# Optimization experiments

Measured on AMD Instinct MI355X. Metric: run time of the kernel, lower is better.

Reference implementation:

```python
import jax, jax.numpy as jnp
import numpy as np

DIM = 512
HEADS = 8


def setup_inputs() -> dict:
    key = jax.random.key(0)
    k1, k2, k3 = jax.random.split(key, 3)
    x = jax.random.normal(k1, (4, DIM, 64, 64), dtype=jnp.float32)
    # kaiming_normal fan_out, linear: std = 1/sqrt(fan_out)
    w_qkv = jax.random.normal(k2, (3 * DIM, DIM), dtype=jnp.float32) / np.sqrt(3 * DIM)
    b_qkv = jnp.zeros((3 * DIM,), dtype=jnp.float32)
    w_proj = jax.random.normal(k3, (DIM, DIM), dtype=jnp.float32) / np.sqrt(DIM)
    b_proj = jnp.zeros((DIM,), dtype=jnp.float32)
    return {"x": x, "w_qkv": w_qkv, "b_qkv": b_qkv, "w_proj": w_proj, "b_proj": b_proj}


def reference(x, w_qkv, b_qkv, w_proj, b_proj):
    B, C, H, W = x.shape
    N = H * W
    hd = C // HEADS
    scale = hd ** -0.5
    x_flat = x.reshape(B, C, N).transpose(0, 2, 1)          # [B, N, C]
    qkv = x_flat @ w_qkv.T + b_qkv                           # [B, N, 3C]
    q, k, v = jnp.split(qkv, 3, axis=-1)
    q = q.reshape(B, N, HEADS, hd).transpose(0, 2, 1, 3)     # [B, h, N, d]
    k = k.reshape(B, N, HEADS, hd).transpose(0, 2, 1, 3)
    v = v.reshape(B, N, HEADS, hd).transpose(0, 2, 1, 3)
    attn = jnp.einsum('bhnd,bhmd->bhnm', q, k) * scale       # [B, h, N, N]
    attn = jnp.clip(attn, -10.0, 10.0)
    attn = jax.nn.softmax(attn, axis=-1)
    out = jnp.einsum('bhnm,bhmd->bhnd', attn, v)             # [B, h, N, d]
    out = out.transpose(0, 2, 1, 3).reshape(B, N, C)         # [B, N, C]
    out = out @ w_proj.T + b_proj
    out = out.transpose(0, 2, 1).reshape(B, C, H, W)
    return x + out
```

## Files before the change

### kernel.cpp

```cpp
#include <hip/hip_runtime.h>

typedef float f32x4 __attribute__((ext_vector_type(4)));
typedef __bf16 bf16x8 __attribute__((ext_vector_type(8)));
typedef unsigned short u16;
typedef unsigned int u32;
typedef u16 u16x4 __attribute__((ext_vector_type(4)));
typedef u16 u16x8 __attribute__((ext_vector_type(8)));

#define DEV static __device__ __forceinline__

constexpr int B = 4, C = 512, NH = 8, HD = 64, NN = 4096, C3 = 1536;
constexpr float K_PRESCALE = 0.125f * 1.4426950408889634f;
constexpr float CLIP2 = 10.0f * 1.4426950408889634f;

DEV u16 f2bf(float f) { union { __bf16 b; u16 s; } u; u.b = (__bf16)f; return u.s; }

__global__ __launch_bounds__(256) void k_transpose(const float* __restrict__ x,
                                                   u16* __restrict__ Xt) {
  __shared__ float tile[64][65];
  const int n0 = blockIdx.x * 64, c0 = blockIdx.y * 64, b = blockIdx.z;
  const int t = threadIdx.x;
  const int cl = t >> 4, n4 = (t & 15) * 4;
#pragma unroll
  for (int rep = 0; rep < 4; ++rep) {
    const int c = rep * 16 + cl;
    const f32x4 v = *(const f32x4*)(x + ((size_t)(b * C + c0 + c)) * NN + n0 + n4);
#pragma unroll
    for (int j = 0; j < 4; ++j) tile[c][n4 + j] = v[j];
  }
  __syncthreads();
#pragma unroll
  for (int rep = 0; rep < 16; ++rep) {
    const int n = rep * 4 + (t >> 6);
    const int c = t & 63;
    Xt[((size_t)(b * NN + n0 + n)) * C + c0 + c] = f2bf(tile[c][n]);
  }
}

__global__ __launch_bounds__(256) void k_cvtw(const float* __restrict__ wq,
                                              const float* __restrict__ wp,
                                              u16* __restrict__ Wq, u16* __restrict__ Wp) {
  const int idx = blockIdx.x * 256 + threadIdx.x;
  const int NQ = C3 * C / 4;
  const float* src;
  u16* dst;
  int i4;
  if (idx < NQ) { src = wq; dst = Wq; i4 = idx; }
  else          { src = wp; dst = Wp; i4 = idx - NQ; }
  const f32x4 v = *(const f32x4*)(src + (size_t)i4 * 4);
  u16x4 o;
#pragma unroll
  for (int j = 0; j < 4; ++j) o[j] = f2bf(v[j]);
  *(u16x4*)(dst + (size_t)i4 * 4) = o;
}

__global__ __launch_bounds__(256) void k_qkv(const u16* __restrict__ Xt,
                                             const u16* __restrict__ W,
                                             const float* __restrict__ bias,
                                             u16* __restrict__ Q, u16* __restrict__ Kq,
                                             u16* __restrict__ Vt) {
  __shared__ u16 smem[16384];
  u16* Alds = smem;
  u16* Blds = smem + 8192;
  const int nt = blockIdx.x, mt = blockIdx.y, b = blockIdx.z;
  const int t = threadIdx.x, w = t >> 6, l = t & 63;
  const int l15 = l & 15, l4 = l >> 4;
  const int wr = w >> 1, wc = w & 1;
  f32x4 acc[4][4] = {};
  const u16* Abase = Xt + (size_t)(b * NN + nt * 128) * C;
  const u16* Bbase = W + (size_t)(mt * 128) * C;

  for (int kt = 0; kt < C / 64; ++kt) {
    __syncthreads();
#pragma unroll
    for (int i = 0; i < 4; ++i) {
      const int cch = t + 256 * i;
      const int r = cch >> 3, kb = (cch & 7) * 16;
      const int sw = kb ^ ((r & 7) << 4);
      *(f32x4*)((char*)Alds + r * 128 + sw) =
          *(const f32x4*)((const char*)(Abase + (size_t)r * C + kt * 64) + kb);
      *(f32x4*)((char*)Blds + r * 128 + sw) =
          *(const f32x4*)((const char*)(Bbase + (size_t)r * C + kt * 64) + kb);
    }
    __syncthreads();
#pragma unroll
    for (int ks = 0; ks < 2; ++ks) {
      bf16x8 af[4], bfr[4];
#pragma unroll
      for (int ri = 0; ri < 4; ++ri) {
        const int row = wr * 64 + ri * 16 + l15;
        af[ri] = *(const bf16x8*)((const char*)Alds + row * 128 +
                                  ((ks * 64 + l4 * 16) ^ ((row & 7) << 4)));
      }
#pragma unroll
      for (int cj = 0; cj < 4; ++cj) {
        const int row = wc * 64 + cj * 16 + l15;
        bfr[cj] = *(const bf16x8*)((const char*)Blds + row * 128 +
                                   ((ks * 64 + l4 * 16) ^ ((row & 7) << 4)));
      }
#pragma unroll
      for (int ri = 0; ri < 4; ++ri)
#pragma unroll
        for (int cj = 0; cj < 4; ++cj)
          acc[ri][cj] = __builtin_amdgcn_mfma_f32_16x16x32_bf16(af[ri], bfr[cj], acc[ri][cj], 0, 0, 0);
    }
  }

  __syncthreads();
  const int sec = mt >> 2;
  const int mtl = mt & 3;
  if (sec < 2) {
#pragma unroll
    for (int ri = 0; ri < 4; ++ri)
#pragma unroll
      for (int cj = 0; cj < 4; ++cj) {
        const int m_l = wc * 64 + cj * 16 + l15;
        const float bv = bias[mt * 128 + m_l];
        const float sc = (sec == 1) ? K_PRESCALE : 1.0f;
#pragma unroll
        for (int r = 0; r < 4; ++r) {
          const int n_l = wr * 64 + ri * 16 + l4 * 4 + r;
          *(u16*)((char*)smem + n_l * 256 + ((m_l * 2) ^ ((n_l & 7) << 4))) =
              f2bf((acc[ri][cj][r] + bv) * sc);
        }
      }
    __syncthreads();
    u16* dst = (sec == 0) ? Q : Kq;
#pragma unroll
    for (int rep = 0; rep < 8; ++rep) {
      const int idx = rep * 256 + t;
      const int n_l = idx >> 4, ch = idx & 15;
      const u16x8 v = *(const u16x8*)((char*)smem + n_l * 256 + ((ch * 16) ^ ((n_l & 7) << 4)));
      const int hh = mtl * 2 + (ch >> 3), dd = (ch & 7) * 8;
      *(u16x8*)(dst + ((size_t)(b * NH + hh) * NN + nt * 128 + n_l) * HD + dd) = v;
    }
  } else {
#pragma unroll
    for (int ri = 0; ri < 4; ++ri)
#pragma unroll
      for (int cj = 0; cj < 4; ++cj) {
        const int m_l = wc * 64 + cj * 16 + l15;
        const float bv = bias[mt * 128 + m_l];
        const int nb = wr * 64 + ri * 16 + l4 * 4;
        u16x4 pv;
#pragma unroll
        for (int r = 0; r < 4; ++r) pv[r] = f2bf(acc[ri][cj][r] + bv);
        *(u16x4*)((char*)smem + m_l * 256 + ((nb * 2) ^ ((m_l & 7) << 4))) = pv;
      }
    __syncthreads();
#pragma unroll
    for (int rep = 0; rep < 8; ++rep) {
      const int idx = rep * 256 + t;
      const int m_l = idx >> 4, ch = idx & 15;
      const u16x8 v = *(const u16x8*)((char*)smem + m_l * 256 + ((ch * 16) ^ ((m_l & 7) << 4)));
      const int hh = mtl * 2 + (m_l >> 6), dd = m_l & 63;
      *(u16x8*)(Vt + ((size_t)(b * NH + hh) * HD + dd) * NN + nt * 128 + ch * 8) = v;
    }
  }
}

__global__ __launch_bounds__(256) void k_attn(const u16* __restrict__ Q,
                                              const u16* __restrict__ K,
                                              const u16* __restrict__ Vt,
                                              u16* __restrict__ AO) {
  __shared__ u16 Klds[4096];
  __shared__ u16 Vlds[4096];
  __shared__ u16 Plds[4096];
  const int qt = blockIdx.x, h = blockIdx.y, b = blockIdx.z;
  const int bh = b * NH + h;
  const int t = threadIdx.x, w = t >> 6, l = t & 63;
  const int l15 = l & 15, l4 = l >> 4;
  const int q0 = qt * 64;

  const u16* qb = Q + ((size_t)bh * NN + q0 + w * 16 + l15) * HD + l4 * 8;
  bf16x8 qf[2];
  qf[0] = *(const bf16x8*)(qb);
  qf[1] = *(const bf16x8*)(qb + 32);

  f32x4 o[4] = {};
  float rs[4] = {};

  const int sr = t >> 3, scb = (t & 7) * 16;
  const int ssw = scb ^ ((sr & 7) << 4);
  char* kwp = (char*)Klds + sr * 128 + ssw;
  char* vwp = (char*)Vlds + sr * 128 + ssw;
  const char* kg = (const char*)(K + (size_t)bh * NN * HD) + sr * 128 + scb;
  const char* vg = (const char*)(Vt + (size_t)bh * HD * NN) + (size_t)sr * 8192 + scb;

  const int sw7 = (l15 & 7) << 4;

  for (int kv = 0; kv < NN / 64; ++kv) {
    __syncthreads();
    *(f32x4*)kwp          = *(const f32x4*)kg;
    *(f32x4*)(kwp + 4096) = *(const f32x4*)(kg + 4096);
    *(f32x4*)vwp          = *(const f32x4*)vg;
    *(f32x4*)(vwp + 4096) = *(const f32x4*)(vg + (size_t)32 * 8192);
    __syncthreads();

    f32x4 s[4] = {};
#pragma unroll
    for (int ks = 0; ks < 2; ++ks) {
#pragma unroll
      for (int cj = 0; cj < 4; ++cj) {
        const bf16x8 kf = *(const bf16x8*)((const char*)Klds + (cj * 16 + l15) * 128 +
                                           ((ks * 64 + l4 * 16) ^ sw7));
        s[cj] = __builtin_amdgcn_mfma_f32_16x16x32_bf16(qf[ks], kf, s[cj], 0, 0, 0);
      }
    }
#pragma unroll
    for (int cj = 0; cj < 4; ++cj) {
      const int colb = (cj * 16 + l15) * 2;
#pragma unroll
      for (int r = 0; r < 4; ++r) {
        const float p = exp2f(fminf(fmaxf(s[cj][r], -CLIP2), CLIP2));
        rs[r] += p;
        const int row = w * 16 + l4 * 4 + r;
        *(u16*)((char*)Plds + row * 128 + (colb ^ ((row & 7) << 4))) = f2bf(p);
      }
    }
    __syncthreads();

#pragma unroll
    for (int ks = 0; ks < 2; ++ks) {
      const int prow = w * 16 + l15;
      const bf16x8 pa = *(const bf16x8*)((const char*)Plds + prow * 128 +
                                         ((ks * 64 + l4 * 16) ^ sw7));
#pragma unroll
      for (int cj = 0; cj < 4; ++cj) {
        const bf16x8 vf = *(const bf16x8*)((const char*)Vlds + (cj * 16 + l15) * 128 +
                                           ((ks * 64 + l4 * 16) ^ sw7));
        o[cj] = __builtin_amdgcn_mfma_f32_16x16x32_bf16(pa, vf, o[cj], 0, 0, 0);
      }
    }
    kg += 8192;
    vg += 128;
  }

#pragma unroll
  for (int r = 0; r < 4; ++r) {
    float v = rs[r];
    v += __shfl_xor(v, 1);
    v += __shfl_xor(v, 2);
    v += __shfl_xor(v, 4);
    v += __shfl_xor(v, 8);
    rs[r] = v;
  }
#pragma unroll
  for (int cj = 0; cj < 4; ++cj)
#pragma unroll
    for (int r = 0; r < 4; ++r) {
      const int n = q0 + w * 16 + l4 * 4 + r;
      const int c = h * 64 + cj * 16 + l15;
      AO[((size_t)(b * NN + n)) * C + c] = f2bf(o[cj][r] / rs[r]);
    }
}

__global__ __launch_bounds__(256) void k_proj(const u16* __restrict__ AO,
                                              const u16* __restrict__ Wp,
                                              const float* __restrict__ bias,
                                              const float* __restrict__ x,
                                              float* __restrict__ out) {
  __shared__ u16 smem[16384];
  u16* Alds = smem;
  u16* Blds = smem + 8192;
  const int nt = blockIdx.x, ct = blockIdx.y, b = blockIdx.z;
  const int t = threadIdx.x, w = t >> 6, l = t & 63;
  const int l15 = l & 15, l4 = l >> 4;
  const int wr = w >> 1, wc = w & 1;
  f32x4 acc[4][4] = {};
  const u16* Abase = AO + (size_t)(b * NN + nt * 128) * C;
  const u16* Bbase = Wp + (size_t)(ct * 128) * C;

  for (int kt = 0; kt < C / 64; ++kt) {
    __syncthreads();
#pragma unroll
    for (int i = 0; i < 4; ++i) {
      const int cch = t + 256 * i;
      const int r = cch >> 3, kb = (cch & 7) * 16;
      const int sw = kb ^ ((r & 7) << 4);
      *(f32x4*)((char*)Alds + r * 128 + sw) =
          *(const f32x4*)((const char*)(Abase + (size_t)r * C + kt * 64) + kb);
      *(f32x4*)((char*)Blds + r * 128 + sw) =
          *(const f32x4*)((const char*)(Bbase + (size_t)r * C + kt * 64) + kb);
    }
    __syncthreads();
#pragma unroll
    for (int ks = 0; ks < 2; ++ks) {
      bf16x8 af[4], bfr[4];
#pragma unroll
      for (int ri = 0; ri < 4; ++ri) {
        const int row = wr * 64 + ri * 16 + l15;
        af[ri] = *(const bf16x8*)((const char*)Alds + row * 128 +
                                  ((ks * 64 + l4 * 16) ^ ((row & 7) << 4)));
      }
#pragma unroll
      for (int cj = 0; cj < 4; ++cj) {
        const int row = wc * 64 + cj * 16 + l15;
        bfr[cj] = *(const bf16x8*)((const char*)Blds + row * 128 +
                                   ((ks * 64 + l4 * 16) ^ ((row & 7) << 4)));
      }
#pragma unroll
      for (int ri = 0; ri < 4; ++ri)
#pragma unroll
        for (int cj = 0; cj < 4; ++cj)
          acc[ri][cj] = __builtin_amdgcn_mfma_f32_16x16x32_bf16(af[ri], bfr[cj], acc[ri][cj], 0, 0, 0);
    }
  }

  float* fs = (float*)smem;
  __syncthreads();
#pragma unroll
  for (int p = 0; p < 2; ++p) {
    if (p) __syncthreads();
    if (wc == p) {
#pragma unroll
      for (int ri = 0; ri < 4; ++ri)
#pragma unroll
        for (int cj = 0; cj < 4; ++cj) {
          const int co = cj * 16 + l15;
          const float bv = bias[ct * 128 + p * 64 + co];
          const int nb = wr * 64 + ri * 16 + l4 * 4;
          f32x4 vv;
#pragma unroll
          for (int r = 0; r < 4; ++r) vv[r] = acc[ri][cj][r] + bv;
          *(f32x4*)((char*)fs + co * 512 + ((nb * 4) ^ ((co & 7) << 4))) = vv;
        }
    }
    __syncthreads();
#pragma unroll
    for (int rep = 0; rep < 8; ++rep) {
      const int idx = rep * 256 + t;
      const int co = idx >> 5, ch = idx & 31;
      f32x4 vv = *(const f32x4*)((char*)fs + co * 512 + ((ch * 16) ^ ((co & 7) << 4)));
      const size_t base = ((size_t)(b * C + ct * 128 + p * 64 + co)) * NN + nt * 128 + ch * 4;
      const f32x4 xr = *(const f32x4*)(x + base);
#pragma unroll
      for (int r = 0; r < 4; ++r) vv[r] += xr[r];
      *(f32x4*)(out + base) = vv;
    }
  }
}

extern "C" void kernel_launch(void* const* d_in, const int* in_sizes, int n_in,
                              void* d_out, int out_size, void* d_ws, size_t ws_size,
                              hipStream_t stream) {
  const float* x      = (const float*)d_in[0];
  const float* w_qkv  = (const float*)d_in[1];
  const float* b_qkv  = (const float*)d_in[2];
  const float* w_proj = (const float*)d_in[3];
  const float* b_proj = (const float*)d_in[4];
  float* out = (float*)d_out;
  char* ws = (char*)d_ws;

  const size_t SZ_XT = (size_t)B * NN * C * 2;
  const size_t SZ_WQ = (size_t)C3 * C * 2;
  const size_t SZ_WP = (size_t)C * C * 2;
  const size_t SZ_QK = (size_t)B * NH * NN * HD * 2;

  u16* Xt = (u16*)(ws);
  u16* Wq = (u16*)(ws + SZ_XT);
  u16* Wp = (u16*)(ws + SZ_XT + SZ_WQ);
  u16* Qb = (u16*)(ws + SZ_XT + SZ_WQ + SZ_WP);
  u16* Kb = (u16*)(ws + SZ_XT + SZ_WQ + SZ_WP + SZ_QK);
  u16* Vt = (u16*)(ws + SZ_XT + SZ_WQ + SZ_WP + 2 * SZ_QK);
  u16* AO = Xt;

  k_transpose<<<dim3(NN / 64, C / 64, B), 256, 0, stream>>>(x, Xt);
  k_cvtw<<<dim3((C3 * C + C * C) / 4 / 256), 256, 0, stream>>>(w_qkv, w_proj, Wq, Wp);
  k_qkv<<<dim3(NN / 128, C3 / 128, B), 256, 0, stream>>>(Xt, Wq, b_qkv, Qb, Kb, Vt);
  k_attn<<<dim3(NN / 64, NH, B), 256, 0, stream>>>(Qb, Kb, Vt, AO);
  k_proj<<<dim3(NN / 128, C / 128, B), 256, 0, stream>>>(AO, Wp, b_proj, x, out);
}
```

Before: 433.8 us.

## Prefetch next KV tile into registers and compute row sums via MFMA

```diff
diff --git a/kernel.cpp b/kernel.cpp
--- a/kernel.cpp
+++ b/kernel.cpp
@@ -14,6 +14,18 @@
 constexpr float CLIP2 = 10.0f * 1.4426950408889634f;
 
 DEV u16 f2bf(float f) { union { __bf16 b; u16 s; } u; u.b = (__bf16)f; return u.s; }
+
+#if __has_builtin(__builtin_amdgcn_exp2f)
+DEV float fast_exp2(float x) { return __builtin_amdgcn_exp2f(x); }
+#else
+DEV float fast_exp2(float x) { return __expf(x * 0.6931471805599453f); }
+#endif
+
+#if __has_builtin(__builtin_amdgcn_fmed3f)
+DEV float clamp2(float x) { return __builtin_amdgcn_fmed3f(x, -CLIP2, CLIP2); }
+#else
+DEV float clamp2(float x) { return fminf(fmaxf(x, -CLIP2), CLIP2); }
+#endif
 
 __global__ __launch_bounds__(256) void k_transpose(const float* __restrict__ x,
                                                    u16* __restrict__ Xt) {
@@ -177,8 +189,14 @@
   qf[0] = *(const bf16x8*)(qb);
   qf[1] = *(const bf16x8*)(qb + 32);
 
+  union { u16 s; __bf16 b; } ob;
+  ob.s = 0x3F80;
+  bf16x8 ones;
+#pragma unroll
+  for (int j = 0; j < 8; ++j) ones[j] = ob.b;
+
   f32x4 o[4] = {};
-  float rs[4] = {};
+  f32x4 rsa = {};
 
   const int sr = t >> 3, scb = (t & 7) * 16;
   const int ssw = scb ^ ((sr & 7) << 4);
@@ -189,13 +207,26 @@
 
   const int sw7 = (l15 & 7) << 4;
 
-  for (int kv = 0; kv < NN / 64; ++kv) {
-    __syncthreads();
-    *(f32x4*)kwp          = *(const f32x4*)kg;
-    *(f32x4*)(kwp + 4096) = *(const f32x4*)(kg + 4096);
-    *(f32x4*)vwp          = *(const f32x4*)vg;
-    *(f32x4*)(vwp + 4096) = *(const f32x4*)(vg + (size_t)32 * 8192);
-    __syncthreads();
+  f32x4 kr0 = *(const f32x4*)kg;
+  f32x4 kr1 = *(const f32x4*)(kg + 4096);
+  f32x4 vr0 = *(const f32x4*)vg;
+  f32x4 vr1 = *(const f32x4*)(vg + (size_t)32 * 8192);
+  *(f32x4*)kwp = kr0;
+  *(f32x4*)(kwp + 4096) = kr1;
+  *(f32x4*)vwp = vr0;
+  *(f32x4*)(vwp + 4096) = vr1;
+  __syncthreads();
+
+  constexpr int NT = NN / 64;
+  for (int kv = 0; kv < NT; ++kv) {
+    if (kv + 1 < NT) {
+      kg += 8192;
+      vg += 128;
+      kr0 = *(const f32x4*)kg;
+      kr1 = *(const f32x4*)(kg + 4096);
+      vr0 = *(const f32x4*)vg;
+      vr1 = *(const f32x4*)(vg + (size_t)32 * 8192);
+    }
 
     f32x4 s[4] = {};
 #pragma unroll
@@ -212,8 +243,7 @@
       const int colb = (cj * 16 + l15) * 2;
 #pragma unroll
       for (int r = 0; r < 4; ++r) {
-        const float p = exp2f(fminf(fmaxf(s[cj][r], -CLIP2), CLIP2));
-        rs[r] += p;
+        const float p = fast_exp2(clamp2(s[cj][r]));
         const int row = w * 16 + l4 * 4 + r;
         *(u16*)((char*)Plds + row * 128 + (colb ^ ((row & 7) << 4))) = f2bf(p);
       }
@@ -231,27 +261,29 @@
                                            ((ks * 64 + l4 * 16) ^ sw7));
         o[cj] = __builtin_amdgcn_mfma_f32_16x16x32_bf16(pa, vf, o[cj], 0, 0, 0);
       }
-    }
-    kg += 8192;
-    vg += 128;
-  }
-
-#pragma unroll
-  for (int r = 0; r < 4; ++r) {
-    float v = rs[r];
-    v += __shfl_xor(v, 1);
-    v += __shfl_xor(v, 2);
-    v += __shfl_xor(v, 4);
-    v += __shfl_xor(v, 8);
-    rs[r] = v;
-  }
+      rsa = __builtin_amdgcn_mfma_f32_16x16x32_bf16(pa, ones, rsa, 0, 0, 0);
+    }
+    __syncthreads();
+
+    if (kv + 1 < NT) {
+      *(f32x4*)kwp = kr0;
+      *(f32x4*)(kwp + 4096) = kr1;
+      *(f32x4*)vwp = vr0;
+      *(f32x4*)(vwp + 4096) = vr1;
+    }
+    __syncthreads();
+  }
+
+  float inv[4];
+#pragma unroll
+  for (int r = 0; r < 4; ++r) inv[r] = 1.0f / rsa[r];
 #pragma unroll
   for (int cj = 0; cj < 4; ++cj)
 #pragma unroll
     for (int r = 0; r < 4; ++r) {
       const int n = q0 + w * 16 + l4 * 4 + r;
       const int c = h * 64 + cj * 16 + l15;
-      AO[((size_t)(b * NN + n)) * C + c] = f2bf(o[cj][r] / rs[r]);
+      AO[((size_t)(b * NN + n)) * C + c] = f2bf(o[cj][r] * inv[r]);
     }
 }
 
```

New measurement: 369.6 us. 1.17x faster.
